# Optimization experiments

Measured on AMD Instinct MI355X. Metric: run time of the kernel, lower is better.

Reference implementation:

```python
import jax, jax.numpy as jnp
import numpy as np

BS, C, H, W = 2, 256, 64, 64
CH = C // 8  # hidden channels = 32


def conv1(x, w, b):
    # 1x1 conv: w [out,in], b [out], x [b,in,H,W] -> [b,out,H,W]
    return jnp.einsum('oc,bchw->bohw', w, x) + b[None, :, None, None]


def setup_inputs() -> dict:
    key = jax.random.key(0)
    ks = jax.random.split(key, 32)
    d = {}
    d['x'] = jax.random.normal(ks[0], (BS, C, H, W), dtype=jnp.float32)
    d['y'] = jax.random.normal(ks[1], (BS, C, H, W), dtype=jnp.float32)
    i = 2
    def wproj(shape):
        nonlocal i
        w = jax.random.normal(ks[i], shape, dtype=jnp.float32) * 0.05
        i += 1
        return w
    for nm in ['f1', 'g1', 'h1', 'f2', 'g2', 'h2']:
        d['w' + nm] = wproj((CH, C))
        d['b' + nm] = jnp.zeros((CH,), dtype=jnp.float32)
    for nm in ['v11', 'v12', 'v21', 'v22']:
        d['w' + nm] = wproj((C, CH))
        d['b' + nm] = jnp.zeros((C,), dtype=jnp.float32)
    for nm in ['o1', 'o2']:
        d['w' + nm] = wproj((C, 2 * C))
        d['b' + nm] = jnp.zeros((C,), dtype=jnp.float32)
    return d


def reference(x, y, wf1, bf1, wg1, bg1, wh1, bh1, wf2, bf2, wg2, bg2, wh2, bh2,
              wv11, bv11, wv12, bv12, wv21, bv21, wv22, bv22, wo1, bo1, wo2, bo2):
    bs, c, h, w = x.shape
    n = h * w
    f1 = conv1(x, wf1, bf1).reshape(bs, -1, n)  # [b,ch,n]
    g1 = conv1(x, wg1, bg1).reshape(bs, -1, n)
    f2 = conv1(y, wf2, bf2).reshape(bs, -1, n)
    g2 = conv1(y, wg2, bg2).reshape(bs, -1, n)
    # attn = softmax(f^T g) over last dim, [b,n,n]
    attn11 = jax.nn.softmax(jnp.einsum('bcn,bcm->bnm', f1, g1), axis=-1)
    attn12 = jax.nn.softmax(jnp.einsum('bcn,bcm->bnm', f1, g2), axis=-1)
    attn21 = jax.nn.softmax(jnp.einsum('bcn,bcm->bnm', f2, g1), axis=-1)
    attn22 = jax.nn.softmax(jnp.einsum('bcn,bcm->bnm', f2, g2), axis=-1)
    h1 = conv1(x, wh1, bh1).reshape(bs, -1, n)  # note: both h from x, as in source
    h2 = conv1(x, wh2, bh2).reshape(bs, -1, n)
    # bmm(h, attn^T): out[c,m] = sum_n h[c,n] attn[m,n]
    v11 = conv1(jnp.einsum('bcn,bmn->bcm', h1, attn11).reshape(bs, -1, h, w), wv11, bv11)
    v12 = conv1(jnp.einsum('bcn,bmn->bcm', h2, attn12).reshape(bs, -1, h, w), wv12, bv12)
    v21 = conv1(jnp.einsum('bcn,bmn->bcm', h1, attn21).reshape(bs, -1, h, w), wv21, bv21)
    v22 = conv1(jnp.einsum('bcn,bmn->bcm', h2, attn22).reshape(bs, -1, h, w), wv22, bv22)
    x_out = x + conv1(jnp.concatenate([v11, v12], axis=1), wo1, bo1)
    y_out = y + conv1(jnp.concatenate([v21, v22], axis=1), wo2, bo2)
    return (x_out, y_out)
```

## Files before the change

kernel.cpp:

```cpp
#include <hip/hip_runtime.h>
#include <hip/hip_bf16.h>
#include <cstdint>

#define N 4096
#define CC 256
#define CH 32
#define L2E 1.4426950408889634f

typedef __attribute__((ext_vector_type(8)))  short short8;
typedef __attribute__((ext_vector_type(16))) float f32x16;
typedef __attribute__((ext_vector_type(4)))  uint32_t u32x4;

#define OFF_WFRAG 0
#define OFF_WEFF  311296
#define OFF_BEFF  344064
#define OFF_QF    344576
#define OFF_KF    606720
#define OFF_VF    868864

__device__ __forceinline__ uint32_t cvtpk_bf16(float lo, float hi) {
  uint32_t r;
  asm("v_cvt_pk_bf16_f32 %0, %1, %2" : "=v"(r) : "v"(lo), "v"(hi));
  return r;
}
__device__ __forceinline__ float bf2f(uint16_t u) {
  return __builtin_bit_cast(float, (uint32_t)u << 16);
}

__device__ __forceinline__ void rows_to_frags(const float* p, u32x4& lo, u32x4& hi) {
#pragma unroll
  for (int kh = 0; kh < 2; ++kh) {
    int base = kh * 8;
    uint32_t x0 = cvtpk_bf16(p[base + 0], p[base + 1]);
    uint32_t y0 = cvtpk_bf16(p[base + 4], p[base + 5]);
    asm volatile("v_permlane32_swap_b32 %0, %1" : "+v"(x0), "+v"(y0));
    uint32_t x1 = cvtpk_bf16(p[base + 2], p[base + 3]);
    uint32_t y1 = cvtpk_bf16(p[base + 6], p[base + 7]);
    asm volatile("v_permlane32_swap_b32 %0, %1" : "+v"(x1), "+v"(y1));
    u32x4 r; r[0] = x0; r[1] = x1; r[2] = y0; r[3] = y1;
    if (kh == 0) lo = r; else hi = r;
  }
}

__device__ __forceinline__ void attn_step(short8 ak0, short8 ak1, short8 bv0, short8 bv1,
                                          short8 bq0, short8 bq1,
                                          f32x16& ao, float& lacc, const f32x16& zero16) {
  __builtin_amdgcn_s_setprio(1);
  f32x16 sa = __builtin_amdgcn_mfma_f32_32x32x16_bf16(ak0, bq0, zero16, 0, 0, 0);
  sa = __builtin_amdgcn_mfma_f32_32x32x16_bf16(ak1, bq1, sa, 0, 0, 0);
  __builtin_amdgcn_s_setprio(0);
  float p[16];
#pragma unroll
  for (int r = 0; r < 16; ++r) p[r] = __builtin_amdgcn_exp2f(sa[r]);
  float t0 = 0.f, t1 = 0.f;
#pragma unroll
  for (int r = 0; r < 8; ++r) { t0 += p[2 * r]; t1 += p[2 * r + 1]; }
  lacc += t0 + t1;
  u32x4 lo, hi;
  rows_to_frags(p, lo, hi);
  __builtin_amdgcn_s_setprio(1);
  ao = __builtin_amdgcn_mfma_f32_32x32x16_bf16(__builtin_bit_cast(short8, lo), bv0, ao, 0, 0, 0);
  ao = __builtin_amdgcn_mfma_f32_32x32x16_bf16(__builtin_bit_cast(short8, hi), bv1, ao, 0, 0, 0);
  __builtin_amdgcn_s_setprio(0);
}

__global__ void k_prep2(const float* __restrict__ wf1, const float* __restrict__ wg1,
                        const float* __restrict__ wh1, const float* __restrict__ wf2,
                        const float* __restrict__ wg2, const float* __restrict__ wh2,
                        const float* __restrict__ wo1, const float* __restrict__ wo2,
                        const float* __restrict__ wv11, const float* __restrict__ wv12,
                        const float* __restrict__ wv21, const float* __restrict__ wv22,
                        const float* __restrict__ bv11, const float* __restrict__ bv12,
                        const float* __restrict__ bv21, const float* __restrict__ bv22,
                        const float* __restrict__ bo1, const float* __restrict__ bo2,
                        uint16_t* __restrict__ wfragb, float* __restrict__ weff,
                        float* __restrict__ beff) {
  int bid = blockIdx.x;
  if (bid < 192) {
    int idx = bid * 256 + threadIdx.x;
    int q = idx >> 13, kb = (idx >> 9) & 15, l = (idx >> 3) & 63, j = idx & 7;
    int ch = l & 31, c = kb * 16 + (l >> 5) * 8 + j;
    const float* w = q == 0 ? wf1 : q == 1 ? wg1 : q == 2 ? wh1
                   : q == 3 ? wf2 : q == 4 ? wg2 : wh2;
    wfragb[idx] = (uint16_t)cvtpk_bf16(w[ch * CC + c], 0.f);
  } else if (bid < 320) {
    int bid2 = bid - 192;
    int r = bid2 >> 6, ch = bid2 & 63, half = ch >> 5, chp = ch & 31;
    int o = threadIdx.x;
    const float* wv = (r == 0) ? (half ? wv12 : wv11) : (half ? wv22 : wv21);
    const float* wrow = (r == 0 ? wo1 : wo2) + (size_t)o * 512 + half * 256;
    float a[8];
#pragma unroll
    for (int u = 0; u < 8; ++u) a[u] = 0.f;
#pragma unroll 4
    for (int c = 0; c < 256; c += 8) {
#pragma unroll
      for (int u = 0; u < 8; ++u)
        a[u] = fmaf(wrow[c + u], wv[(c + u) * CH + chp], a[u]);
    }
    weff[((size_t)r * 64 + ch) * 256 + o] =
        ((a[0] + a[1]) + (a[2] + a[3])) + ((a[4] + a[5]) + (a[6] + a[7]));
  } else {
    int r = bid - 320;
    int o = threadIdx.x;
    const float* bo  = r == 0 ? bo1 : bo2;
    const float* bva = r == 0 ? bv11 : bv21;
    const float* bvb = r == 0 ? bv12 : bv22;
    const float* wrow = (r == 0 ? wo1 : wo2) + (size_t)o * 512;
    float a[4], b4[4];
#pragma unroll
    for (int u = 0; u < 4; ++u) { a[u] = 0.f; b4[u] = 0.f; }
#pragma unroll 8
    for (int c = 0; c < 256; c += 4) {
#pragma unroll
      for (int u = 0; u < 4; ++u) {
        a[u]  = fmaf(wrow[c + u],       bva[c + u], a[u]);
        b4[u] = fmaf(wrow[c + u + 256], bvb[c + u], b4[u]);
      }
    }
    beff[r * 256 + o] = bo[o] + ((a[0] + a[1]) + (a[2] + a[3]))
                              + ((b4[0] + b4[1]) + (b4[2] + b4[3]));
  }
}

__global__ __launch_bounds__(256) void k_proj(
    const float* __restrict__ x, const float* __restrict__ y,
    const uint16_t* __restrict__ wfragb,
    const float* __restrict__ bf1, const float* __restrict__ bg1, const float* __restrict__ bh1,
    const float* __restrict__ bf2, const float* __restrict__ bg2, const float* __restrict__ bh2,
    uint16_t* __restrict__ Qf, uint16_t* __restrict__ Kf, uint16_t* __restrict__ Vf) {
  __shared__ float xch[2][64][17];
  int bid = blockIdx.x;
  int w = __builtin_amdgcn_readfirstlane(threadIdx.x >> 6);
  int l = threadIdx.x & 63, l31 = l & 31, l5 = l >> 5;

  int q, ql, b, nt, inst, khalf, pair;
  const float* src;
  const float* bias;
  bool isf, isV;
  if (bid < 512) {
    int chunk = bid >> 1;
    ql = (bid & 1) * 2 + (w >> 1); khalf = w & 1; pair = w >> 1;
    b = chunk >> 7; nt = chunk & 127;
    src = x; inst = 0;
    q = (ql == 3) ? 5 : ql;
    isf = (ql == 0); isV = (ql >= 2);
    bias = ql == 0 ? bf1 : ql == 1 ? bg1 : ql == 2 ? bh1 : bh2;
  } else {
    int u = (bid - 512) * 4 + w;
    int task = u >> 1; khalf = u & 1; pair = w >> 1;
    int chunk = task >> 1; ql = task & 1;
    b = chunk >> 7; nt = chunk & 127;
    src = y; inst = 1;
    q = 3 + ql;
    isf = (ql == 0); isV = false;
    bias = ql == 0 ? bf2 : bg2;
  }

  const u32x4* wp = (const u32x4*)wfragb + (size_t)q * 16 * 64 + (size_t)khalf * 8 * 64 + l;
  u32x4 wfr[8];
#pragma unroll
  for (int kb = 0; kb < 8; ++kb) wfr[kb] = wp[kb * 64];

  const float* sp = src + (size_t)b * CC * N + (size_t)(khalf * 128 + l5 * 8) * N + nt * 32 + l31;
  f32x16 acc;
#pragma unroll
  for (int r = 0; r < 16; ++r) acc[r] = 0.f;

  if (isV) {
#pragma unroll
    for (int kb = 0; kb < 8; ++kb) {
      const float* kp = sp + (size_t)kb * 16 * N;
      float xj[8];
#pragma unroll
      for (int j = 0; j < 8; ++j) xj[j] = kp[(size_t)j * N];
      u32x4 bu;
#pragma unroll
      for (int jh = 0; jh < 4; ++jh) bu[jh] = cvtpk_bf16(xj[2 * jh], xj[2 * jh + 1]);
      acc = __builtin_amdgcn_mfma_f32_32x32x16_bf16(
          __builtin_bit_cast(short8, bu), __builtin_bit_cast(short8, wfr[kb]), acc, 0, 0, 0);
    }
  } else {
#pragma unroll
    for (int kb = 0; kb < 8; ++kb) {
      const float* kp = sp + (size_t)kb * 16 * N;
      float xj[8];
#pragma unroll
      for (int j = 0; j < 8; ++j) xj[j] = kp[(size_t)j * N];
      u32x4 bu;
#pragma unroll
      for (int jh = 0; jh < 4; ++jh) bu[jh] = cvtpk_bf16(xj[2 * jh], xj[2 * jh + 1]);
      acc = __builtin_amdgcn_mfma_f32_32x32x16_bf16(
          __builtin_bit_cast(short8, wfr[kb]), __builtin_bit_cast(short8, bu), acc, 0, 0, 0);
    }
  }

  if (khalf == 1) {
#pragma unroll
    for (int r = 0; r < 16; ++r) xch[pair][l][r] = acc[r];
  }
  __syncthreads();
  if (khalf == 1) return;
#pragma unroll
  for (int r = 0; r < 16; ++r) acc[r] += xch[pair][l][r];

  float p[16];
  if (isV) {
    float bv = bias[l31];
#pragma unroll
    for (int r = 0; r < 16; ++r) p[r] = acc[r] + bv;
  } else {
#pragma unroll
    for (int r = 0; r < 16; ++r) {
      int crow = (r & 3) + 8 * (r >> 2) + 4 * l5;
      float t = acc[r] + bias[crow];
      p[r] = isf ? t * L2E : t;
    }
  }

  u32x4 lo, hi;
  rows_to_frags(p, lo, hi);

  uint16_t* dstb = isV ? Vf : (isf ? Qf : Kf);
  int oinst = isV ? (ql - 2) : inst;
  int b128 = (oinst * 2 + b) * 128 + nt;
  uint32_t* d0 = (uint32_t*)dstb + (size_t)b128 * 512 + l * 4;
  *(u32x4*)d0 = lo;
  *(u32x4*)(d0 + 256) = hi;
}

__global__ __launch_bounds__(512) void k_attnepi(const uint16_t* __restrict__ Qf,
                                                 const uint16_t* __restrict__ Kf,
                                                 const uint16_t* __restrict__ Vf,
                                                 const float* __restrict__ x,
                                                 const float* __restrict__ y,
                                                 const float* __restrict__ weff,
                                                 const float* __restrict__ beff,
                                                 float* __restrict__ out) {
  __shared__ uint16_t redAO[2][2][4][32][34];
  __shared__ float    redL[2][2][4][32];
  __shared__ uint16_t AN[64][66];
  int bid = blockIdx.x;
  int qg = bid & 63, rb = bid >> 6, r = rb >> 1, b = rb & 1;
  int tid = threadIdx.x;
  int w = __builtin_amdgcn_readfirstlane(tid >> 6);
  int ik = w >> 2, kw = w & 3;
  int l = tid & 63, l31 = l & 31, l5 = l >> 5;
  int qt0 = qg * 2, qt1 = qg * 2 + 1;

  const uint16_t* Qp0 = Qf + (size_t)((r * 2 + b) * 128 + qt0) * 1024 + l * 8;
  const uint16_t* Qp1 = Qf + (size_t)((r * 2 + b) * 128 + qt1) * 1024 + l * 8;
  const uint16_t* Kp = Kf + (size_t)((ik * 2 + b) * 128 + kw * 32) * 1024 + l * 8;
  const uint16_t* Vp = Vf + (size_t)((ik * 2 + b) * 128 + kw * 32) * 1024 + l * 8;

  short8 bq00 = *(const short8*)(Qp0);
  short8 bq01 = *(const short8*)(Qp0 + 512);
  short8 bq10 = *(const short8*)(Qp1);
  short8 bq11 = *(const short8*)(Qp1 + 512);

  f32x16 zero16, ao0, ao1;
#pragma unroll
  for (int rr = 0; rr < 16; ++rr) { zero16[rr] = 0.f; ao0[rr] = 0.f; ao1[rr] = 0.f; }
  float lacc0 = 0.f, lacc1 = 0.f;

  for (int t = 0; t < 32; ++t) {
    const uint16_t* kt = Kp + t * 1024;
    short8 ak0 = *(const short8*)(kt);
    short8 ak1 = *(const short8*)(kt + 512);
    const uint16_t* vt = Vp + t * 1024;
    short8 bv0 = *(const short8*)(vt);
    short8 bv1 = *(const short8*)(vt + 512);
    attn_step(ak0, ak1, bv0, bv1, bq00, bq01, ao0, lacc0, zero16);
    attn_step(ak0, ak1, bv0, bv1, bq10, bq11, ao1, lacc1, zero16);
  }

#pragma unroll
  for (int rr = 0; rr < 16; ++rr) {
    int row = (rr & 3) + 8 * (rr >> 2) + 4 * l5;
    redAO[ik][0][kw][row][l31] = (uint16_t)cvtpk_bf16(ao0[rr], ao0[rr]);
    redAO[ik][1][kw][row][l31] = (uint16_t)cvtpk_bf16(ao1[rr], ao1[rr]);
  }
  lacc0 += __shfl_xor(lacc0, 32);
  lacc1 += __shfl_xor(lacc1, 32);
  if (l < 32) {
    redL[ik][0][kw][l31] = lacc0;
    redL[ik][1][kw][l31] = lacc1;
  }
  __syncthreads();

  {
    int ch = tid >> 3, mblk = tid & 7;
    int qi = mblk >> 2, mq0 = (mblk & 3) * 8;
    int ikc = ch >> 5, chp = ch & 31;
#pragma unroll
    for (int mm = 0; mm < 8; ++mm) {
      int mq = mq0 + mm;
      float L = redL[ikc][qi][0][mq] + redL[ikc][qi][1][mq]
              + redL[ikc][qi][2][mq] + redL[ikc][qi][3][mq];
      float s = bf2f(redAO[ikc][qi][0][mq][chp]) + bf2f(redAO[ikc][qi][1][mq][chp])
              + bf2f(redAO[ikc][qi][2][mq][chp]) + bf2f(redAO[ikc][qi][3][mq][chp]);
      float v = s * __builtin_amdgcn_rcpf(L);
      AN[ch][qi * 32 + mq] = (uint16_t)cvtpk_bf16(v, v);
    }
  }
  __syncthreads();

  int m = tid & 63;
  int m0 = qg * 64;
  float acc[32];
#pragma unroll
  for (int j = 0; j < 32; ++j) acc[j] = 0.f;
  const float* wrow = weff + (size_t)(r * 64) * 256 + w * 32;
  for (int ch = 0; ch < 64; ++ch) {
    float a = bf2f(AN[ch][m]);
    const float* wr = wrow + (size_t)ch * 256;
#pragma unroll
    for (int j = 0; j < 32; ++j) acc[j] = fmaf(wr[j], a, acc[j]);
  }
  const float* src = r == 0 ? x : y;
  float* outr = out + (size_t)r * 2 * CC * N;
  const float* be = beff + r * 256 + w * 32;
#pragma unroll
  for (int j = 0; j < 32; ++j) {
    size_t off = ((size_t)b * CC + w * 32 + j) * N + m0 + m;
    outr[off] = src[off] + acc[j] + be[j];
  }
}

extern "C" void kernel_launch(void* const* d_in, const int* in_sizes, int n_in,
                              void* d_out, int out_size, void* d_ws, size_t ws_size,
                              hipStream_t stream) {
  const float* x    = (const float*)d_in[0];
  const float* y    = (const float*)d_in[1];
  const float* wf1  = (const float*)d_in[2];
  const float* bf1  = (const float*)d_in[3];
  const float* wg1  = (const float*)d_in[4];
  const float* bg1  = (const float*)d_in[5];
  const float* wh1  = (const float*)d_in[6];
  const float* bh1  = (const float*)d_in[7];
  const float* wf2  = (const float*)d_in[8];
  const float* bf2  = (const float*)d_in[9];
  const float* wg2  = (const float*)d_in[10];
  const float* bg2  = (const float*)d_in[11];
  const float* wh2  = (const float*)d_in[12];
  const float* bh2  = (const float*)d_in[13];
  const float* wv11 = (const float*)d_in[14];
  const float* bv11 = (const float*)d_in[15];
  const float* wv12 = (const float*)d_in[16];
  const float* bv12 = (const float*)d_in[17];
  const float* wv21 = (const float*)d_in[18];
  const float* bv21 = (const float*)d_in[19];
  const float* wv22 = (const float*)d_in[20];
  const float* bv22 = (const float*)d_in[21];
  const float* wo1  = (const float*)d_in[22];
  const float* bo1  = (const float*)d_in[23];
  const float* wo2  = (const float*)d_in[24];
  const float* bo2  = (const float*)d_in[25];

  float* ws   = (float*)d_ws;
  uint16_t* wfragb = (uint16_t*)(ws + OFF_WFRAG);
  float* weff = ws + OFF_WEFF;
  float* beff = ws + OFF_BEFF;
  uint16_t* Qf = (uint16_t*)(ws + OFF_QF);
  uint16_t* Kf = (uint16_t*)(ws + OFF_KF);
  uint16_t* Vf = (uint16_t*)(ws + OFF_VF);
  float* out  = (float*)d_out;

  k_prep2<<<322, 256, 0, stream>>>(wf1, wg1, wh1, wf2, wg2, wh2, wo1, wo2,
                                   wv11, wv12, wv21, wv22,
                                   bv11, bv12, bv21, bv22, bo1, bo2,
                                   wfragb, weff, beff);
  k_proj<<<768, 256, 0, stream>>>(x, y, wfragb, bf1, bg1, bh1, bf2, bg2, bh2, Qf, Kf, Vf);
  k_attnepi<<<256, 512, 0, stream>>>(Qf, Kf, Vf, x, y, weff, beff, out);
}
```

Before: 68.32 us.

## Software-pipeline K/V fragment loads and split accumulators in attention loop

The attention main loop now processes two key tiles per iteration with independent accumulator sets, and prefetches the next pair of K/V fragments into registers before running the current MFMA steps. The aim is to hide global-load latency and break the dependency chain on a single accumulator. The launch bound also gains a minimum of two blocks per CU, which caps register use. The extra prefetch registers and duplicated accumulators raise register pressure and could cause spills under that cap. The wrap-around prefetch on the last iteration also issues one redundant load.

```diff
diff --git a/kernel.cpp b/kernel.cpp
--- a/kernel.cpp
+++ b/kernel.cpp
@@ -229,14 +229,14 @@
   *(u32x4*)(d0 + 256) = hi;
 }
 
-__global__ __launch_bounds__(512) void k_attnepi(const uint16_t* __restrict__ Qf,
-                                                 const uint16_t* __restrict__ Kf,
-                                                 const uint16_t* __restrict__ Vf,
-                                                 const float* __restrict__ x,
-                                                 const float* __restrict__ y,
-                                                 const float* __restrict__ weff,
-                                                 const float* __restrict__ beff,
-                                                 float* __restrict__ out) {
+__global__ __launch_bounds__(512, 2) void k_attnepi(const uint16_t* __restrict__ Qf,
+                                                    const uint16_t* __restrict__ Kf,
+                                                    const uint16_t* __restrict__ Vf,
+                                                    const float* __restrict__ x,
+                                                    const float* __restrict__ y,
+                                                    const float* __restrict__ weff,
+                                                    const float* __restrict__ beff,
+                                                    float* __restrict__ out) {
   __shared__ uint16_t redAO[2][2][4][32][34];
   __shared__ float    redL[2][2][4][32];
   __shared__ uint16_t AN[64][66];
@@ -258,21 +258,45 @@
   short8 bq10 = *(const short8*)(Qp1);
   short8 bq11 = *(const short8*)(Qp1 + 512);
 
-  f32x16 zero16, ao0, ao1;
-#pragma unroll
-  for (int rr = 0; rr < 16; ++rr) { zero16[rr] = 0.f; ao0[rr] = 0.f; ao1[rr] = 0.f; }
-  float lacc0 = 0.f, lacc1 = 0.f;
-
-  for (int t = 0; t < 32; ++t) {
-    const uint16_t* kt = Kp + t * 1024;
-    short8 ak0 = *(const short8*)(kt);
-    short8 ak1 = *(const short8*)(kt + 512);
-    const uint16_t* vt = Vp + t * 1024;
-    short8 bv0 = *(const short8*)(vt);
-    short8 bv1 = *(const short8*)(vt + 512);
-    attn_step(ak0, ak1, bv0, bv1, bq00, bq01, ao0, lacc0, zero16);
-    attn_step(ak0, ak1, bv0, bv1, bq10, bq11, ao1, lacc1, zero16);
-  }
+  f32x16 zero16, ao0a, ao0b, ao1a, ao1b;
+#pragma unroll
+  for (int rr = 0; rr < 16; ++rr) {
+    zero16[rr] = 0.f; ao0a[rr] = 0.f; ao0b[rr] = 0.f; ao1a[rr] = 0.f; ao1b[rr] = 0.f;
+  }
+  float lacc0a = 0.f, lacc0b = 0.f, lacc1a = 0.f, lacc1b = 0.f;
+
+  short8 akA0 = *(const short8*)(Kp);
+  short8 akA1 = *(const short8*)(Kp + 512);
+  short8 bvA0 = *(const short8*)(Vp);
+  short8 bvA1 = *(const short8*)(Vp + 512);
+  short8 akB0 = *(const short8*)(Kp + 1024);
+  short8 akB1 = *(const short8*)(Kp + 1536);
+  short8 bvB0 = *(const short8*)(Vp + 1024);
+  short8 bvB1 = *(const short8*)(Vp + 1536);
+  for (int t = 0; t < 32; t += 2) {
+    int tn = (t + 2) & 31;
+    const uint16_t* nk = Kp + tn * 1024;
+    const uint16_t* nv = Vp + tn * 1024;
+    short8 nakA0 = *(const short8*)(nk);
+    short8 nakA1 = *(const short8*)(nk + 512);
+    short8 nbvA0 = *(const short8*)(nv);
+    short8 nbvA1 = *(const short8*)(nv + 512);
+    short8 nakB0 = *(const short8*)(nk + 1024);
+    short8 nakB1 = *(const short8*)(nk + 1536);
+    short8 nbvB0 = *(const short8*)(nv + 1024);
+    short8 nbvB1 = *(const short8*)(nv + 1536);
+    attn_step(akA0, akA1, bvA0, bvA1, bq00, bq01, ao0a, lacc0a, zero16);
+    attn_step(akA0, akA1, bvA0, bvA1, bq10, bq11, ao1a, lacc1a, zero16);
+    attn_step(akB0, akB1, bvB0, bvB1, bq00, bq01, ao0b, lacc0b, zero16);
+    attn_step(akB0, akB1, bvB0, bvB1, bq10, bq11, ao1b, lacc1b, zero16);
+    akA0 = nakA0; akA1 = nakA1; bvA0 = nbvA0; bvA1 = nbvA1;
+    akB0 = nakB0; akB1 = nakB1; bvB0 = nbvB0; bvB1 = nbvB1;
+  }
+
+  f32x16 ao0, ao1;
+#pragma unroll
+  for (int rr = 0; rr < 16; ++rr) { ao0[rr] = ao0a[rr] + ao0b[rr]; ao1[rr] = ao1a[rr] + ao1b[rr]; }
+  float lacc0 = lacc0a + lacc0b, lacc1 = lacc1a + lacc1b;
 
 #pragma unroll
   for (int rr = 0; rr < 16; ++rr) {
```

New measurement: 66.69 us. 2.4% less time.
